# Kernel optimization log

Hardware: AMD Instinct MI355X
Metric: run time of the kernel (lower is better)

The kernel has to match this reference:

```python
import jax, jax.numpy as jnp
import numpy as np

RADIUS = 0.2
K = 32
H_RES = 480
W_RES = 640
DIM = 128
EPS = 1e-5  # BatchNorm2d default eps


def setup_inputs() -> dict:
    key = jax.random.key(0)
    k1, k2, k3 = jax.random.split(key, 3)
    B, N = 2, 4096
    xyzp = jax.random.normal(k1, (B, N, 4), jnp.float32)
    features = jax.random.normal(k2, (B, N, DIM), jnp.float32)
    Wm = jax.random.normal(k3, (2 * DIM + 9, DIM), jnp.float32) * 0.05
    b = jnp.zeros((DIM,), jnp.float32)
    gamma = jnp.ones((DIM,), jnp.float32)
    beta = jnp.zeros((DIM,), jnp.float32)
    return {"xyzp": xyzp, "features": features, "Wm": Wm, "b": b, "gamma": gamma, "beta": beta}


def _ball_query(xyz, radius, k):
    # pytorch3d-style ball query: first k point indices (in index order) within radius, pad -1
    B, N, _ = xyz.shape
    d2 = jnp.sum((xyz[:, :, None, :] - xyz[:, None, :, :]) ** 2, axis=-1)  # [B,N,N]
    mask = d2 < radius * radius
    keyv = jnp.where(mask, jnp.arange(N)[None, None, :], N)
    order = jnp.argsort(keyv, axis=-1)[:, :, :k]  # stable sort -> first indices within radius
    count = mask.sum(axis=-1)
    return jnp.where(jnp.arange(k)[None, None, :] < count[:, :, None], order, -1)


def _knn_gather(x, idx):
    # x: [B,N,C], idx: [B,N,K] -> [B,N,K,C]
    B, N, Kk = idx.shape
    flat = idx.reshape(B, N * Kk)
    return jnp.take_along_axis(x, flat[:, :, None], axis=1).reshape(B, N, Kk, x.shape[-1])


def reference(xyzp, features, Wm, b, gamma, beta):
    B, N, _ = xyzp.shape
    # detached xyz with z (time) zeroed, used only for neighbor search
    xyz = jax.lax.stop_gradient(xyzp[..., :3]).at[..., 2].set(0.0)
    idx = _ball_query(xyz, RADIUS, K)
    self_idx = jnp.broadcast_to(jnp.arange(N)[None, :, None], (B, N, K))
    idx = jnp.where(idx == -1, self_idx, idx)

    d = xyzp[:, :, None, :] - _knn_gather(xyzp, idx)  # [B,N,K,4]
    ts = d[..., 2:3]
    ts = jnp.where(ts == 0, jnp.float32(1e-6), ts)
    res = jnp.array([W_RES, H_RES], jnp.float32)
    speed = d[..., :2] / ts * res  # [B,N,K,2]
    mean_speed = jnp.broadcast_to(speed.mean(axis=(1, 2), keepdims=True), speed.shape)
    p = jnp.abs(d[..., 3:4])

    knn_f = _knn_gather(features, idx)  # [B,N,K,DIM]
    f0 = jnp.broadcast_to(features[:, :, None, :], (B, N, K, features.shape[-1]))
    f = jnp.concatenate([f0, knn_f, d, speed, p, mean_speed], axis=-1)  # [B,N,K,2*DIM+9]

    h = f @ Wm + b  # Linear
    # BatchNorm2d in training mode: per-channel stats over (B,N,K)
    mu = h.mean(axis=(0, 1, 2))
    var = h.var(axis=(0, 1, 2))
    h = (h - mu) / jnp.sqrt(var + EPS) * gamma + beta
    h = jax.nn.relu(h)
    return h.max(axis=-2)  # max over K neighbors -> [B,N,DIM]
```

## Files before the change

### kernel.cpp

```cpp
#include <hip/hip_runtime.h>
#include <math.h>

#define NB   2
#define NP   4096
#define KNN  32
#define DIMC 128
#define NROWS (NB*NP)
#define MTOT  (NB*NP*KNN)
#define K2BLOCKS 512
#define MAINBLOCKS 512

static constexpr float R2 = 0.04f;

__global__ __launch_bounds__(256) void k1(const float* __restrict__ feat,
                                          const float* __restrict__ Wm,
                                          float* __restrict__ e,
                                          float* __restrict__ g)
{
    __shared__ float sa[32*132];
    const int t      = threadIdx.x;
    const int rowblk = blockIdx.x >> 2;
    const int colblk = blockIdx.x & 3;
    const int cb     = colblk >> 1;
    const int coff   = (colblk & 1) * 64;
    const int row0   = rowblk * 32;
    const int tr     = t >> 4;
    const int tc     = t & 15;
    const float* wsrc = Wm + (size_t)cb*128*DIMC + coff;

    #pragma unroll
    for (int q = 0; q < 4; ++q) {
        const int fid = q*256 + t;
        const int r   = fid >> 5;
        const int kq  = fid & 31;
        const float4 v = *(const float4*)(feat + (size_t)(row0 + r)*DIMC + kq*4);
        *(float4*)&sa[r*132 + kq*4] = v;
    }
    __syncthreads();

    float acc[2][4];
    #pragma unroll
    for (int i = 0; i < 2; ++i) { acc[i][0]=0.f; acc[i][1]=0.f; acc[i][2]=0.f; acc[i][3]=0.f; }

    #pragma unroll 2
    for (int k4 = 0; k4 < 32; ++k4) {
        float4 bw[4];
        #pragma unroll
        for (int j = 0; j < 4; ++j)
            bw[j] = *(const float4*)(wsrc + (size_t)(k4*4 + j)*DIMC + tc*4);
        float4 ar[2];
        ar[0] = *(const float4*)&sa[(2*tr    )*132 + k4*4];
        ar[1] = *(const float4*)&sa[(2*tr + 1)*132 + k4*4];
        #pragma unroll
        for (int j = 0; j < 4; ++j) {
            #pragma unroll
            for (int i = 0; i < 2; ++i) {
                const float a = (j==0)?ar[i].x:(j==1)?ar[i].y:(j==2)?ar[i].z:ar[i].w;
                acc[i][0] = fmaf(a, bw[j].x, acc[i][0]);
                acc[i][1] = fmaf(a, bw[j].y, acc[i][1]);
                acc[i][2] = fmaf(a, bw[j].z, acc[i][2]);
                acc[i][3] = fmaf(a, bw[j].w, acc[i][3]);
            }
        }
    }

    float* dst = cb ? g : e;
    #pragma unroll
    for (int i = 0; i < 2; ++i)
        *(float4*)(dst + (size_t)(row0 + 2*tr + i)*DIMC + coff + tc*4) =
            make_float4(acc[i][0], acc[i][1], acc[i][2], acc[i][3]);
}

__global__ __launch_bounds__(256) void k2(const float* __restrict__ xyzp,
                                          const float* __restrict__ e,
                                          const float* __restrict__ g,
                                          const float* __restrict__ Wm,
                                          const float* __restrict__ bbias,
                                          double* __restrict__ spart,
                                          float* __restrict__ hmaxA,
                                          float* __restrict__ hminA,
                                          float* __restrict__ stpartT)
{
    __shared__ float xy[NP*2];
    __shared__ int   idxrow[16*KNN];
    __shared__ float geo[4][2][KNN][8];
    __shared__ float l1s[8][DIMC];
    __shared__ float l2s[8][DIMC];
    __shared__ float swr[8];

    const int bx  = blockIdx.x;
    const int xcd = bx & 7;
    const int pb  = ((xcd >> 2) << 8) + (bx >> 3)*4 + (xcd & 3);
    const int b   = pb >> 8;
    const int p0  = (pb & 255) * 16;

    const int t    = threadIdx.x;
    const int w    = t >> 6;
    const int lane = t & 63;
    const float* xb = xyzp + (size_t)b*NP*4;

    for (int q = t; q < NP; q += 256) {
        const float4 v = *(const float4*)(xb + (size_t)q*4);
        xy[q*2 + 0] = v.x;
        xy[q*2 + 1] = v.y;
    }
    __syncthreads();

    const int pl0 = p0 + w*4;
    unsigned long long wacc[4] = {0ULL, 0ULL, 0ULL, 0ULL};
    {
#pragma clang fp contract(off)
        float xi[4], yi[4];
        #pragma unroll
        for (int p = 0; p < 4; ++p) { xi[p] = xy[(pl0+p)*2]; yi[p] = xy[(pl0+p)*2+1]; }
        for (int c = 0; c < NP/64; ++c) {
            const float2 q = *(const float2*)(xy + (size_t)(c*64 + lane)*2);
            const bool keep = (lane == c);
            #pragma unroll
            for (int p = 0; p < 4; ++p) {
                const float dx = xi[p] - q.x;
                const float dy = yi[p] - q.y;
                const float dx2 = dx*dx;
                const float dy2 = dy*dy;
                const unsigned long long m = __ballot((dx2 + dy2) < R2);
                if (keep) wacc[p] = m;
            }
        }
    }

    #pragma unroll
    for (int p = 0; p < 4; ++p) {
        unsigned long long wd = wacc[p];
        const int cnt = __popcll(wd);
        int pre = cnt;
        #pragma unroll
        for (int off = 1; off < 64; off <<= 1) {
            const int tv = __shfl_up(pre, off);
            if (lane >= off) pre += tv;
        }
        const int total = __shfl(pre, 63);
        int slot = pre - cnt;
        unsigned long long ww = wd;
        while (ww != 0ULL && slot < KNN) {
            const int bpos = __builtin_ctzll(ww);
            idxrow[(w*4 + p)*KNN + slot] = lane*64 + bpos;
            ww &= ww - 1ULL;
            ++slot;
        }
        const int iself = pl0 + p;
        for (int kk = min(total, KNN) + lane; kk < KNN; kk += 64)
            idxrow[(w*4 + p)*KNN + kk] = iself;
    }

    const int half = lane >> 5;
    const int lq   = lane & 31;
    const int c0   = lq * 4;
    float4 w2r[7];
    #pragma unroll
    for (int r = 0; r < 7; ++r)
        w2r[r] = *(const float4*)(Wm + (size_t)(256 + r)*DIMC + c0);
    const float4 bb4 = *(const float4*)(bbias + c0);

    float s1x=0.f,s1y=0.f,s1z=0.f,s1w=0.f;
    float s2x=0.f,s2y=0.f,s2z=0.f,s2w=0.f;
    float sxacc = 0.f, syacc = 0.f;
    const float* gbb = g + (size_t)b*NP*DIMC + c0;

    for (int rp = 0; rp < 2; ++rp) {
        const int rloc = w*4 + rp*2 + half;
        const int ptl  = p0 + rloc;
        const int j0   = idxrow[rloc*KNN + lq];
        const float4 pj = *(const float4*)(xb + (size_t)j0*4);
        const float4 pi = *(const float4*)(xb + (size_t)ptl*4);
        const float dx = pi.x - pj.x;
        const float dy = pi.y - pj.y;
        const float dz = pi.z - pj.z;
        const float dwv = pi.w - pj.w;
        const float ts  = (dz == 0.f) ? 1e-6f : dz;
        const float rts = __builtin_amdgcn_rcpf(ts);
        const float sxv = dx*rts*640.f;
        const float syv = dy*rts*480.f;
        *(float4*)&geo[w][half][lq][0] = make_float4(dx, dy, dz, dwv);
        *(float4*)&geo[w][half][lq][4] = make_float4(sxv, syv, fabsf(dwv), __int_as_float(j0));
        sxacc += sxv; syacc += syv;
        __builtin_amdgcn_wave_barrier();

        const size_t rowg = (size_t)b*NP + ptl;
        const float4 ee = *(const float4*)(e + rowg*DIMC + c0);
        const float ecx = ee.x + bb4.x, ecy = ee.y + bb4.y;
        const float ecz = ee.z + bb4.z, ecw = ee.w + bb4.w;
        float mxx=-INFINITY,mxy=-INFINITY,mxz=-INFINITY,mxw=-INFINITY;
        float mnx= INFINITY,mny= INFINITY,mnz= INFINITY,mnw= INFINITY;
        #pragma unroll 4
        for (int k = 0; k < KNN; ++k) {
            const float4 g0 = *(const float4*)&geo[w][half][k][0];
            const float4 g1 = *(const float4*)&geo[w][half][k][4];
            const int jj = __float_as_int(g1.w);
            const float4 gg = *(const float4*)(gbb + (size_t)jj*DIMC);

            float h0 = ecx + gg.x;
            h0 = fmaf(g0.x, w2r[0].x, h0); h0 = fmaf(g0.y, w2r[1].x, h0);
            h0 = fmaf(g0.z, w2r[2].x, h0); h0 = fmaf(g0.w, w2r[3].x, h0);
            h0 = fmaf(g1.x, w2r[4].x, h0); h0 = fmaf(g1.y, w2r[5].x, h0);
            h0 = fmaf(g1.z, w2r[6].x, h0);
            mxx = fmaxf(mxx, h0); mnx = fminf(mnx, h0);
            s1x += h0; s2x = fmaf(h0, h0, s2x);

            float h1 = ecy + gg.y;
            h1 = fmaf(g0.x, w2r[0].y, h1); h1 = fmaf(g0.y, w2r[1].y, h1);
            h1 = fmaf(g0.z, w2r[2].y, h1); h1 = fmaf(g0.w, w2r[3].y, h1);
            h1 = fmaf(g1.x, w2r[4].y, h1); h1 = fmaf(g1.y, w2r[5].y, h1);
            h1 = fmaf(g1.z, w2r[6].y, h1);
            mxy = fmaxf(mxy, h1); mny = fminf(mny, h1);
            s1y += h1; s2y = fmaf(h1, h1, s2y);

            float h2 = ecz + gg.z;
            h2 = fmaf(g0.x, w2r[0].z, h2); h2 = fmaf(g0.y, w2r[1].z, h2);
            h2 = fmaf(g0.z, w2r[2].z, h2); h2 = fmaf(g0.w, w2r[3].z, h2);
            h2 = fmaf(g1.x, w2r[4].z, h2); h2 = fmaf(g1.y, w2r[5].z, h2);
            h2 = fmaf(g1.z, w2r[6].z, h2);
            mxz = fmaxf(mxz, h2); mnz = fminf(mnz, h2);
            s1z += h2; s2z = fmaf(h2, h2, s2z);

            float h3 = ecw + gg.w;
            h3 = fmaf(g0.x, w2r[0].w, h3); h3 = fmaf(g0.y, w2r[1].w, h3);
            h3 = fmaf(g0.z, w2r[2].w, h3); h3 = fmaf(g0.w, w2r[3].w, h3);
            h3 = fmaf(g1.x, w2r[4].w, h3); h3 = fmaf(g1.y, w2r[5].w, h3);
            h3 = fmaf(g1.z, w2r[6].w, h3);
            mxw = fmaxf(mxw, h3); mnw = fminf(mnw, h3);
            s1w += h3; s2w = fmaf(h3, h3, s2w);
        }
        *(float4*)(hmaxA + rowg*DIMC + c0) = make_float4(mxx, mxy, mxz, mxw);
        *(float4*)(hminA + rowg*DIMC + c0) = make_float4(mnx, mny, mnz, mnw);
        __builtin_amdgcn_wave_barrier();
    }

    #pragma unroll
    for (int off = 32; off > 0; off >>= 1) {
        sxacc += __shfl_down(sxacc, off);
        syacc += __shfl_down(syacc, off);
    }
    if (lane == 0) { swr[w*2] = sxacc; swr[w*2+1] = syacc; }

    *(float4*)&l1s[w*2 + half][c0] = make_float4(s1x, s1y, s1z, s1w);
    *(float4*)&l2s[w*2 + half][c0] = make_float4(s2x, s2y, s2z, s2w);
    __syncthreads();
    if (t < DIMC) {
        float v = 0.f;
        #pragma unroll
        for (int r = 0; r < 8; ++r) v += l1s[r][t];
        stpartT[(size_t)t*MAINBLOCKS + pb] = v;
    } else {
        const int c = t - DIMC;
        float v = 0.f;
        #pragma unroll
        for (int r = 0; r < 8; ++r) v += l2s[r][c];
        stpartT[(size_t)(DIMC + c)*MAINBLOCKS + pb] = v;
    }
    if (t == 0) {
        const double s0 = ((double)swr[0] + (double)swr[2]) + ((double)swr[4] + (double)swr[6]);
        const double s1 = ((double)swr[1] + (double)swr[3]) + ((double)swr[5] + (double)swr[7]);
        spart[(size_t)pb*2 + 0] = s0;
        spart[(size_t)pb*2 + 1] = s1;
    }
}

__global__ __launch_bounds__(256) void kE(const float* __restrict__ stpartT,
                                          const double* __restrict__ spart,
                                          const float* __restrict__ Wm,
                                          const float* __restrict__ gamma,
                                          const float* __restrict__ beta,
                                          float* __restrict__ abuf,
                                          float* __restrict__ dbuf2)
{
    __shared__ double red[256][8];
    const int c = blockIdx.x;
    const int t = threadIdx.x;

    red[t][0] = spart[(size_t)t*2];
    red[t][1] = spart[(size_t)t*2 + 1];
    red[t][2] = spart[(size_t)(t+256)*2];
    red[t][3] = spart[(size_t)(t+256)*2 + 1];
    red[t][4] = (double)stpartT[(size_t)c*MAINBLOCKS + t];
    red[t][5] = (double)stpartT[(size_t)c*MAINBLOCKS + 256 + t];
    red[t][6] = (double)stpartT[(size_t)(c + DIMC)*MAINBLOCKS + t];
    red[t][7] = (double)stpartT[(size_t)(c + DIMC)*MAINBLOCKS + 256 + t];
    __syncthreads();
    for (int st = 128; st > 0; st >>= 1) {
        if (t < st) {
            #pragma unroll
            for (int q = 0; q < 8; ++q) red[t][q] += red[t+st][q];
        }
        __syncthreads();
    }
    if (t == 0) {
        const double NKd = (double)(NP*KNN);
        const float ms0x = (float)(red[0][0] / NKd);
        const float ms0y = (float)(red[0][1] / NKd);
        const float ms1x = (float)(red[0][2] / NKd);
        const float ms1y = (float)(red[0][3] / NKd);
        const float wx = Wm[263*DIMC + c];
        const float wy = Wm[264*DIMC + c];
        const double cb0 = (double)fmaf(ms0x, wx, ms0y*wy);
        const double cb1 = (double)fmaf(ms1x, wx, ms1y*wy);
        const double s1b0 = red[0][4], s1b1 = red[0][5];
        const double s2b0 = red[0][6], s2b1 = red[0][7];
        const double M  = (double)MTOT;
        const double S1 = s1b0 + s1b1 + NKd*(cb0 + cb1);
        const double S2 = (s2b0 + 2.0*cb0*s1b0 + NKd*cb0*cb0)
                        + (s2b1 + 2.0*cb1*s1b1 + NKd*cb1*cb1);
        const double mu  = S1 / M;
        const double var = S2 / M - mu*mu;
        const double inv = 1.0 / sqrt(var + 1e-5);
        const double a  = (double)gamma[c] * inv;
        const double db = (double)beta[c] - mu*a;
        abuf[c] = (float)a;
        dbuf2[c]        = (float)(db + cb0*a);
        dbuf2[DIMC + c] = (float)(db + cb1*a);
    }
}

__global__ __launch_bounds__(256) void kF(const float* __restrict__ hmaxA,
                                          const float* __restrict__ hminA,
                                          const float* __restrict__ abuf,
                                          const float* __restrict__ dbuf2,
                                          float* __restrict__ out)
{
    const int gid = blockIdx.x*256 + threadIdx.x;
    const int row = gid >> 6;
    const int c0  = (gid & 63)*2;
    const int b   = row >> 12;
    const size_t off = (size_t)row*DIMC + c0;
    const float2 mx = *(const float2*)(hmaxA + off);
    const float2 mn = *(const float2*)(hminA + off);
    const float a0 = abuf[c0],  a1 = abuf[c0+1];
    const float d0 = dbuf2[b*DIMC + c0], d1 = dbuf2[b*DIMC + c0 + 1];
    const float h0 = (a0 >= 0.f) ? mx.x : mn.x;
    const float h1 = (a1 >= 0.f) ? mx.y : mn.y;
    float2 o;
    o.x = fmaxf(fmaf(h0, a0, d0), 0.0f);
    o.y = fmaxf(fmaf(h1, a1, d1), 0.0f);
    *(float2*)(out + off) = o;
}

extern "C" void kernel_launch(void* const* d_in, const int* in_sizes, int n_in,
                              void* d_out, int out_size, void* d_ws, size_t ws_size,
                              hipStream_t stream)
{
    const float* xyzp  = (const float*)d_in[0];
    const float* feat  = (const float*)d_in[1];
    const float* Wm    = (const float*)d_in[2];
    const float* bbias = (const float*)d_in[3];
    const float* gamma = (const float*)d_in[4];
    const float* beta  = (const float*)d_in[5];

    char* ws = (char*)d_ws;
    const size_t MB = 1u << 20;
    float*  g       = (float*) (ws + 1*MB);
    float*  e       = (float*) (ws + 5*MB);
    float*  hmaxA   = (float*) (ws + 9*MB);
    float*  hminA   = (float*) (ws + 13*MB);
    double* spart   = (double*)(ws + 17*MB);
    float*  abuf    = (float*) (ws + 17*MB + 65536);
    float*  dbuf2   = (float*) (ws + 17*MB + 66560);
    float*  stpartT = (float*) (ws + 18*MB);

    k1 <<<1024, 256, 0, stream>>>(feat, Wm, e, g);
    k2 <<<K2BLOCKS, 256, 0, stream>>>(xyzp, e, g, Wm, bbias, spart, hmaxA, hminA, stpartT);
    kE <<<DIMC, 256, 0, stream>>>(stpartT, spart, Wm, gamma, beta, abuf, dbuf2);
    kF <<<(NROWS*64)/256, 256, 0, stream>>>(hmaxA, hminA, abuf, dbuf2, (float*)d_out);
}
```

Measured before the change: 58.01 us.

## Restructure feature GEMM as per-wave 8-row tiles with uniform feature loads

Rewrites the k1 projection kernel so each wavefront computes 8 rows by 64 columns. Each lane owns one output column, and feature rows are read with wave-uniform float4 loads instead of being staged through LDS. This removes the shared-memory staging and the __syncthreads barrier. In exchange, weight reuse per load drops, with only 8 rows per weight fetch instead of 32. The launch grid must also match the new work mapping, which is not visible here.

```diff
diff --git a/kernel.cpp b/kernel.cpp
--- a/kernel.cpp
+++ b/kernel.cpp
@@ -17,58 +17,45 @@
                                           float* __restrict__ e,
                                           float* __restrict__ g)
 {
-    __shared__ float sa[32*132];
-    const int t      = threadIdx.x;
-    const int rowblk = blockIdx.x >> 2;
-    const int colblk = blockIdx.x & 3;
-    const int cb     = colblk >> 1;
-    const int coff   = (colblk & 1) * 64;
-    const int row0   = rowblk * 32;
-    const int tr     = t >> 4;
-    const int tc     = t & 15;
-    const float* wsrc = Wm + (size_t)cb*128*DIMC + coff;
-
-    #pragma unroll
-    for (int q = 0; q < 4; ++q) {
-        const int fid = q*256 + t;
-        const int r   = fid >> 5;
-        const int kq  = fid & 31;
-        const float4 v = *(const float4*)(feat + (size_t)(row0 + r)*DIMC + kq*4);
-        *(float4*)&sa[r*132 + kq*4] = v;
-    }
-    __syncthreads();
-
-    float acc[2][4];
-    #pragma unroll
-    for (int i = 0; i < 2; ++i) { acc[i][0]=0.f; acc[i][1]=0.f; acc[i][2]=0.f; acc[i][3]=0.f; }
+    const int t    = threadIdx.x;
+    const int lane = t & 63;
+    const int wid  = __builtin_amdgcn_readfirstlane(t >> 6);
+    const int wgl  = blockIdx.x * 4 + wid;
+    const int row0 = (wgl >> 2) * 8;
+    const int cg   = wgl & 3;
+    const int wbase = (cg >> 1) * 128;
+    const int c0    = (cg & 1) * 64;
+
+    const float* __restrict__ fptr = feat + (size_t)row0 * DIMC;
+    const float* __restrict__ wptr = Wm + (size_t)wbase * DIMC + c0 + lane;
+
+    float acc[8];
+    #pragma unroll
+    for (int r = 0; r < 8; ++r) acc[r] = 0.f;
 
     #pragma unroll 2
     for (int k4 = 0; k4 < 32; ++k4) {
-        float4 bw[4];
+        float bv[4];
         #pragma unroll
         for (int j = 0; j < 4; ++j)
-            bw[j] = *(const float4*)(wsrc + (size_t)(k4*4 + j)*DIMC + tc*4);
-        float4 ar[2];
-        ar[0] = *(const float4*)&sa[(2*tr    )*132 + k4*4];
-        ar[1] = *(const float4*)&sa[(2*tr + 1)*132 + k4*4];
-        #pragma unroll
-        for (int j = 0; j < 4; ++j) {
-            #pragma unroll
-            for (int i = 0; i < 2; ++i) {
-                const float a = (j==0)?ar[i].x:(j==1)?ar[i].y:(j==2)?ar[i].z:ar[i].w;
-                acc[i][0] = fmaf(a, bw[j].x, acc[i][0]);
-                acc[i][1] = fmaf(a, bw[j].y, acc[i][1]);
-                acc[i][2] = fmaf(a, bw[j].z, acc[i][2]);
-                acc[i][3] = fmaf(a, bw[j].w, acc[i][3]);
-            }
-        }
-    }
-
-    float* dst = cb ? g : e;
-    #pragma unroll
-    for (int i = 0; i < 2; ++i)
-        *(float4*)(dst + (size_t)(row0 + 2*tr + i)*DIMC + coff + tc*4) =
-            make_float4(acc[i][0], acc[i][1], acc[i][2], acc[i][3]);
+            bv[j] = wptr[(size_t)(k4*4 + j)*DIMC];
+        float4 as[8];
+        #pragma unroll
+        for (int r = 0; r < 8; ++r)
+            as[r] = *(const float4*)(fptr + (size_t)r*DIMC + k4*4);
+        #pragma unroll
+        for (int r = 0; r < 8; ++r) {
+            acc[r] = fmaf(as[r].x, bv[0], acc[r]);
+            acc[r] = fmaf(as[r].y, bv[1], acc[r]);
+            acc[r] = fmaf(as[r].z, bv[2], acc[r]);
+            acc[r] = fmaf(as[r].w, bv[3], acc[r]);
+        }
+    }
+
+    float* dst = (cg >> 1) ? g : e;
+    #pragma unroll
+    for (int r = 0; r < 8; ++r)
+        dst[(size_t)(row0 + r)*DIMC + c0 + lane] = acc[r];
 }
 
 __global__ __launch_bounds__(256) void k2(const float* __restrict__ xyzp,
```

Result: faster. 53.30 us (-8.1%).
